# Kernel tuning notes

Measured on AMD Instinct MI355X. Metric: run time of the kernel, lower is better.

The kernel has to match this reference:

```python
import jax, jax.numpy as jnp
from jax import lax
import numpy as np

NDIM = 256
BATCH = 65536
NROT = NDIM * (NDIM - 1) // 2  # comb(ndim, 2) = 32640


def _givens_mat(rots, ii, jj, ndim):
    """Product G_last @ ... @ G_1 of Givens rotations in combinations order.

    Left-multiplying by G(i, j, theta) only modifies rows i and j, so we apply
    each rotation as a rank-2 row update instead of a full matmul (same math
    as the original `plane_rot_mat @ mat` loop).
    """
    def step(mat, carry):
        i, j, th = carry
        c = jnp.cos(th)
        s = jnp.sin(th)
        ri = mat[i]
        rj = mat[j]
        mat = mat.at[i].set(c * ri - s * rj)
        mat = mat.at[j].set(s * ri + c * rj)
        return mat, None

    mat0 = jnp.eye(ndim, dtype=jnp.complex64)
    mat, _ = lax.scan(step, mat0, (ii, jj, rots))
    return mat


def setup_inputs() -> dict:
    key = jax.random.key(0)
    k1, k2, k3, k4 = jax.random.split(key, 4)
    x = jax.random.normal(k1, (BATCH, NDIM), dtype=jnp.float32)
    rots1 = 0.1 * jax.random.normal(k2, (NROT,), dtype=jnp.float32)
    phases = 0.1 * jax.random.normal(k3, (NDIM,), dtype=jnp.float32)
    rots2 = 0.1 * jax.random.normal(k4, (NROT,), dtype=jnp.float32)
    return {"x": x, "rots1": rots1, "phases": phases, "rots2": rots2}


def reference(x, rots1, phases, rots2):
    ndim = x.shape[1]
    # np.triu_indices(ndim, 1) enumerates (i, j) pairs in the same row-major
    # order as itertools.combinations(range(ndim), 2).
    ii_np, jj_np = np.triu_indices(ndim, k=1)
    ii = jnp.asarray(ii_np, dtype=jnp.int32)
    jj = jnp.asarray(jj_np, dtype=jnp.int32)

    # vector_norm: row-wise L2 normalization
    xn = x / jnp.linalg.norm(x, axis=1, keepdims=True)
    xc = xn.astype(jnp.complex64)

    # rot1: y = x @ M1.T with M1 = G_last @ ... @ G_1
    M1 = _givens_mat(rots1, ii, jj, ndim)
    y = xc @ M1.T

    # phase_transforms: x @ diag(exp(i*phases)) == elementwise phase multiply
    y = y * jnp.exp(1j * phases)

    # rot2
    M2 = _givens_mat(rots2, ii, jj, ndim)
    y = y @ M2.T

    # measure: |.|^2
    return jnp.abs(y) ** 2
```

## Files before the change

### kernel.cpp

```cpp
#include <hip/hip_runtime.h>
#include <stdint.h>
#include <math.h>

#define NDIM 256
#define BATCH 65536
#define NROT 32640

typedef float  f32x4 __attribute__((ext_vector_type(4)));
typedef short  s16x8 __attribute__((ext_vector_type(8)));
typedef unsigned int u32x4 __attribute__((ext_vector_type(4)));
typedef unsigned int u32x2 __attribute__((ext_vector_type(2)));

static __device__ __forceinline__ unsigned short f2bf(float f) {
    unsigned int u = __float_as_uint(f);
    u += 0x7fffu + ((u >> 16) & 1u);
    return (unsigned short)(u >> 16);
}
static __device__ __forceinline__ float bf2f(unsigned short h) {
    return __uint_as_float(((unsigned)h) << 16);
}

static __device__ __forceinline__ void split4(f32x4 v, u32x2* hi, u32x2* lo) {
    unsigned short h[4], l[4];
    #pragma unroll
    for (int i = 0; i < 4; i++) {
        h[i] = f2bf(v[i]);
        l[i] = f2bf(v[i] - bf2f(h[i]));
    }
    *hi = (u32x2){ (unsigned)h[0] | ((unsigned)h[1] << 16),
                   (unsigned)h[2] | ((unsigned)h[3] << 16) };
    *lo = (u32x2){ (unsigned)l[0] | ((unsigned)l[1] << 16),
                   (unsigned)l[2] | ((unsigned)l[3] << 16) };
}
static __device__ __forceinline__ void split8(const float* v, u32x4* hi, u32x4* lo) {
    unsigned short h[8], l[8];
    #pragma unroll
    for (int i = 0; i < 8; i++) {
        h[i] = f2bf(v[i]);
        l[i] = f2bf(v[i] - bf2f(h[i]));
    }
    *hi = (u32x4){ (unsigned)h[0] | ((unsigned)h[1] << 16),
                   (unsigned)h[2] | ((unsigned)h[3] << 16),
                   (unsigned)h[4] | ((unsigned)h[5] << 16),
                   (unsigned)h[6] | ((unsigned)h[7] << 16) };
    *lo = (u32x4){ (unsigned)l[0] | ((unsigned)l[1] << 16),
                   (unsigned)l[2] | ((unsigned)l[3] << 16),
                   (unsigned)l[4] | ((unsigned)l[5] << 16),
                   (unsigned)l[6] | ((unsigned)l[7] << 16) };
}

static __device__ __forceinline__ int sweep_bound(int k, int pblk) {
    int target = k * (NROT / pblk);
    int best = 0, bd = 0x7fffffff;
    for (int i = 0; i <= 256; i += 4) {
        int pre = i * 255 - (i * (i - 1)) / 2;
        int d = pre - target; d = (d < 0) ? -d : d;
        if (d < bd) { bd = d; best = i; }
    }
    return best;
}

__global__ __launch_bounds__(256) void k_cs(const float* __restrict__ r1,
                                            const float* __restrict__ r2,
                                            float2* __restrict__ cs) {
    int i = blockIdx.x * 256 + threadIdx.x;
    float th = (i < NROT) ? r1[i] : r2[i - NROT];
    float sv, cv; sincosf(th, &sv, &cv);
    cs[i] = make_float2(cv, sv);
}

__global__ __launch_bounds__(64) void k_blocks(const float2* __restrict__ cs,
                                               float* __restrict__ bmats, int pblk) {
    __shared__ float colb[264 * 64];
    __shared__ float2 csb[256 * 4];
    __shared__ float2 tri[24 * 6];

    const int t = threadIdx.x;
    const int bid = blockIdx.x;
    const int chunk = bid & 3;
    const int b = (bid >> 2) % pblk;
    const int set = (bid >> 2) / pblk;
    const int col0 = chunk * 64;
    const float2* cst = cs + (size_t)set * NROT;

    const int s0 = sweep_bound(b, pblk);
    const int s1 = sweep_bound(b + 1, pblk);
    const int ngroups = (s1 - s0) >> 2;

    {
        const f32x4 z = {0.f, 0.f, 0.f, 0.f};
        #pragma unroll 11
        for (int q = 0; q < 66; q++)
            *(f32x4*)&colb[(q * 64 + t) * 4] = z;
        colb[(col0 + t) * 64 + t] = 1.0f;
    }

    for (int k = t; k < ngroups * 6; k += 64) {
        int g = k / 6, q = k - g * 6;
        int a  = (q < 3) ? 0 : ((q < 5) ? 1 : 2);
        int bb = (q < 3) ? (q + 1) : ((q < 5) ? (q - 1) : 3);
        int m0 = s0 + g * 4;
        int m = m0 + a;
        int base = m * 255 - (m * (m - 1)) / 2;
        tri[k] = cst[base - m - 1 + m0 + bb];
    }

    float2 gv[16];
    {
        const int m0g = s0;
        int offg[4];
        #pragma unroll
        for (int a = 0; a < 4; a++) {
            int m = m0g + a;
            offg[a] = m * 255 - (m * (m - 1)) / 2 - m - 1;
        }
        #pragma unroll
        for (int it = 0; it < 16; it++) {
            int k = t + it * 64;
            int jj = k >> 2, a = k & 3;
            int j = m0g + 4 + jj;
            gv[it] = (j < 256) ? cst[offg[a] + j] : make_float2(1.f, 0.f);
        }
        #pragma unroll
        for (int it = 0; it < 16; it++)
            csb[t + it * 64] = gv[it];
    }

    for (int g = 0; g < ngroups; g++) {
        const int m0 = s0 + g * 4;
        const int n_j = 252 - m0;
        const int n_p = (n_j > 0) ? ((n_j + 7) & ~7) : 0;
        const float* csbuf = (const float*)&csb[0];

        const bool have_next = (g + 1 < ngroups);
        if (have_next) {
            const int m0g = m0 + 4;
            int offg[4];
            #pragma unroll
            for (int a = 0; a < 4; a++) {
                int m = m0g + a;
                offg[a] = m * 255 - (m * (m - 1)) / 2 - m - 1;
            }
            #pragma unroll
            for (int it = 0; it < 16; it++) {
                int k = t + it * 64;
                int jj = k >> 2, a = k & 3;
                int j = m0g + 4 + jj;
                gv[it] = (j < 256) ? cst[offg[a] + j] : make_float2(1.f, 0.f);
            }
        }

        float u0 = colb[(m0 + 0) * 64 + t];
        float u1 = colb[(m0 + 1) * 64 + t];
        float u2 = colb[(m0 + 2) * 64 + t];
        float u3 = colb[(m0 + 3) * 64 + t];

        {
            float2 cv; float nr;
            cv = tri[g * 6 + 0]; nr = cv.y * u0 + cv.x * u1; u0 = cv.x * u0 - cv.y * u1; u1 = nr;
            cv = tri[g * 6 + 1]; nr = cv.y * u0 + cv.x * u2; u0 = cv.x * u0 - cv.y * u2; u2 = nr;
            cv = tri[g * 6 + 2]; nr = cv.y * u0 + cv.x * u3; u0 = cv.x * u0 - cv.y * u3; u3 = nr;
            cv = tri[g * 6 + 3]; nr = cv.y * u1 + cv.x * u2; u1 = cv.x * u1 - cv.y * u2; u2 = nr;
            cv = tri[g * 6 + 4]; nr = cv.y * u1 + cv.x * u3; u1 = cv.x * u1 - cv.y * u3; u3 = nr;
            cv = tri[g * 6 + 5]; nr = cv.y * u2 + cv.x * u3; u2 = cv.x * u2 - cv.y * u3; u3 = nr;
        }

        if (n_p > 0) {
            float rbuf[8];
            f32x4 abuf[8][2];
            #pragma unroll
            for (int p = 0; p < 8; p++) {
                rbuf[p] = colb[(m0 + 4 + p) * 64 + t];
                abuf[p][0] = *(const f32x4*)&csbuf[p * 8 + 0];
                abuf[p][1] = *(const f32x4*)&csbuf[p * 8 + 4];
            }
            for (int c = 0; c < n_p; c += 8) {
                #pragma unroll
                for (int p = 0; p < 8; p++) {
                    const int j = m0 + 4 + c + p;
                    float r = rbuf[p];
                    f32x4 A01 = abuf[p][0], A23 = abuf[p][1];
                    int jn = j + 8; jn = (jn < 263) ? jn : 263;
                    int cn = c + p + 8; cn = (cn < n_p) ? cn : (n_p - 1);
                    rbuf[p] = colb[jn * 64 + t];
                    abuf[p][0] = *(const f32x4*)&csbuf[cn * 8 + 0];
                    abuf[p][1] = *(const f32x4*)&csbuf[cn * 8 + 4];
                    float nr;
                    nr = A01[1] * u0 + A01[0] * r; u0 = A01[0] * u0 - A01[1] * r; r = nr;
                    nr = A01[3] * u1 + A01[2] * r; u1 = A01[2] * u1 - A01[3] * r; r = nr;
                    nr = A23[1] * u2 + A23[0] * r; u2 = A23[0] * u2 - A23[1] * r; r = nr;
                    nr = A23[3] * u3 + A23[2] * r; u3 = A23[2] * u3 - A23[3] * r; r = nr;
                    colb[j * 64 + t] = r;
                }
            }
        }
        colb[(m0 + 0) * 64 + t] = u0;
        colb[(m0 + 1) * 64 + t] = u1;
        colb[(m0 + 2) * 64 + t] = u2;
        colb[(m0 + 3) * 64 + t] = u3;

        if (have_next) {
            #pragma unroll
            for (int it = 0; it < 16; it++)
                csb[t + it * 64] = gv[it];
        }
    }

    float* outm = bmats + (size_t)(set * pblk + b) * 65536;
    for (int r = 0; r < 256; r++)
        outm[(size_t)r * 256 + col0 + t] = colb[r * 64 + t];
}

static __device__ __forceinline__ void xnorm_item(const float* __restrict__ xg,
                                                  unsigned short* __restrict__ xbf,
                                                  int id, int tid) {
    const int w = tid >> 6, lane = tid & 63;
    const int r0 = id * 64;
    #pragma unroll 2
    for (int p = 0; p < 16; p++) {
        int row = r0 + p * 4 + w;
        f32x4 v = *(const f32x4*)&xg[(size_t)row * 256 + lane * 4];
        float s = v[0] * v[0] + v[1] * v[1] + v[2] * v[2] + v[3] * v[3];
        #pragma unroll
        for (int off = 32; off; off >>= 1) s += __shfl_xor(s, off, 64);
        float sc = 1.0f / sqrtf(s);
        unsigned short h0 = f2bf(v[0] * sc), h1 = f2bf(v[1] * sc);
        unsigned short h2 = f2bf(v[2] * sc), h3 = f2bf(v[3] * sc);
        u32x2 pk = { (unsigned)h0 | ((unsigned)h1 << 16),
                     (unsigned)h2 | ((unsigned)h3 << 16) };
        *(u32x2*)&xbf[(size_t)row * 256 + lane * 4] = pk;
    }
}

#define TB 2560

static __device__ __forceinline__ int bslot(int row, int s) {
    return row * 40 + ((s ^ ((row >> 3) & 3)) << 3);
}

static __device__ __forceinline__ void tile_issueA(const float* __restrict__ Am,
                                                   int tr, int kb, int tid,
                                                   f32x4 va[2]) {
    #pragma unroll
    for (int it = 0; it < 2; it++) {
        int flat = tid + it * 256;
        int r = flat >> 3, c4 = flat & 7;
        va[it] = *(const f32x4*)&Am[(size_t)(tr * 64 + r) * 256 + kb * 32 + c4 * 4];
    }
}
static __device__ __forceinline__ void tile_issueB(const float* __restrict__ Bm,
                                                   int tc, int kb, int bn, int bkq,
                                                   float vb[8]) {
    #pragma unroll
    for (int i = 0; i < 8; i++)
        vb[i] = Bm[(size_t)(kb * 32 + bkq * 8 + i) * 256 + tc * 64 + bn];
}
static __device__ __forceinline__ void tile_commit(unsigned short* __restrict__ Ahi,
                                                   unsigned short* __restrict__ Alo,
                                                   unsigned short* __restrict__ Bhi,
                                                   unsigned short* __restrict__ Blo,
                                                   int tid, int bn, int bkq,
                                                   const f32x4 va[2], const float vb[8]) {
    #pragma unroll
    for (int it = 0; it < 2; it++) {
        int flat = tid + it * 256;
        int r = flat >> 3, c4 = flat & 7;
        u32x2 hi, lo; split4(va[it], &hi, &lo);
        *(u32x2*)&Ahi[r * 40 + c4 * 4] = hi;
        *(u32x2*)&Alo[r * 40 + c4 * 4] = lo;
    }
    u32x4 hi8, lo8; split8(vb, &hi8, &lo8);
    *(u32x4*)&Bhi[bslot(bn, bkq)] = hi8;
    *(u32x4*)&Blo[bslot(bn, bkq)] = lo8;
}
static __device__ __forceinline__ void tile_mfma(const unsigned short* __restrict__ Ahi,
                                                 const unsigned short* __restrict__ Alo,
                                                 const unsigned short* __restrict__ Bhi,
                                                 const unsigned short* __restrict__ Blo,
                                                 int mh, int nh, int l15, int lq,
                                                 f32x4 acc[2][2]) {
    s16x8 ah[2], al[2], bh[2], bl[2];
    #pragma unroll
    for (int tm = 0; tm < 2; tm++) {
        ah[tm] = *(const s16x8*)&Ahi[(mh + tm * 16 + l15) * 40 + lq * 8];
        al[tm] = *(const s16x8*)&Alo[(mh + tm * 16 + l15) * 40 + lq * 8];
    }
    #pragma unroll
    for (int tn = 0; tn < 2; tn++) {
        bh[tn] = *(const s16x8*)&Bhi[bslot(nh + tn * 16 + l15, lq)];
        bl[tn] = *(const s16x8*)&Blo[bslot(nh + tn * 16 + l15, lq)];
    }
    #pragma unroll
    for (int tm = 0; tm < 2; tm++)
        #pragma unroll
        for (int tn = 0; tn < 2; tn++) {
            acc[tm][tn] = __builtin_amdgcn_mfma_f32_16x16x32_bf16(ah[tm], bh[tn], acc[tm][tn], 0, 0, 0);
            acc[tm][tn] = __builtin_amdgcn_mfma_f32_16x16x32_bf16(ah[tm], bl[tn], acc[tm][tn], 0, 0, 0);
            acc[tm][tn] = __builtin_amdgcn_mfma_f32_16x16x32_bf16(al[tm], bh[tn], acc[tm][tn], 0, 0, 0);
        }
}

static __device__ void combine_tile(const float* __restrict__ src,
                                    float* __restrict__ dst,
                                    int half, int pblk, int bx, int by, int tid,
                                    unsigned short* Ahi, unsigned short* Alo,
                                    unsigned short* Bhi, unsigned short* Blo) {
    const int set = by / half, pidx = by % half;
    const int stride = pblk / (2 * half);
    const int s0A = sweep_bound((2 * pidx + 1) * stride, pblk);
    const float* Am = src + (size_t)(set * 2 * half + 2 * pidx + 1) * 65536;
    const float* Bm = src + (size_t)(set * 2 * half + 2 * pidx) * 65536;
    float* Dm = dst + (size_t)(set * half + pidx) * 65536;
    const int tr = bx >> 2, tc = bx & 3;

    if (tr * 64 + 64 <= s0A) {
        #pragma unroll
        for (int it = 0; it < 4; it++) {
            int flat = tid + it * 256;
            int r = flat >> 4, c4 = flat & 15;
            size_t idx = (size_t)(tr * 64 + r) * 256 + tc * 64 + c4 * 4;
            *(f32x4*)&Dm[idx] = *(const f32x4*)&Bm[idx];
        }
        return;
    }
    const int kb0 = (tr * 64 >= s0A) ? (s0A >> 5) : 0;

    const int lane = tid & 63, w = tid >> 6;
    const int mh = (w >> 1) * 32, nh = (w & 1) * 32;
    const int l15 = lane & 15, lq = lane >> 4;
    const int bn = tid & 63, bkq = tid >> 6;

    f32x4 acc[2][2];
    #pragma unroll
    for (int i = 0; i < 2; i++)
        #pragma unroll
        for (int j = 0; j < 2; j++) acc[i][j] = (f32x4){0.f, 0.f, 0.f, 0.f};

    f32x4 vaE[2], vaO[2]; float vbE[8], vbO[8];
    tile_issueA(Am, tr, kb0, tid, vaE);
    tile_issueB(Bm, tc, kb0, bn, bkq, vbE);
    if (kb0 + 1 < 8) {
        tile_issueA(Am, tr, kb0 + 1, tid, vaO);
        tile_issueB(Bm, tc, kb0 + 1, bn, bkq, vbO);
    }

    for (int kb = kb0; kb < 8; kb++) {
        const int cur = (kb - kb0) & 1;
        if (cur == 0) {
            tile_commit(Ahi, Alo, Bhi, Blo, tid, bn, bkq, vaE, vbE);
            __syncthreads();
            if (kb + 2 < 8) {
                tile_issueA(Am, tr, kb + 2, tid, vaE);
                tile_issueB(Bm, tc, kb + 2, bn, bkq, vbE);
            }
        } else {
            tile_commit(Ahi, Alo, Bhi, Blo, tid, bn, bkq, vaO, vbO);
            __syncthreads();
            if (kb + 2 < 8) {
                tile_issueA(Am, tr, kb + 2, tid, vaO);
                tile_issueB(Bm, tc, kb + 2, bn, bkq, vbO);
            }
        }
        tile_mfma(Ahi, Alo, Bhi, Blo, mh, nh, l15, lq, acc);
        __syncthreads();
    }
    #pragma unroll
    for (int tm = 0; tm < 2; tm++)
        #pragma unroll
        for (int tn = 0; tn < 2; tn++)
            #pragma unroll
            for (int r = 0; r < 4; r++)
                Dm[(size_t)(tr * 64 + mh + tm * 16 + lq * 4 + r) * 256
                   + tc * 64 + nh + tn * 16 + l15] = acc[tm][tn][r];
}

static __device__ void abt_tile(const float* __restrict__ mats,
                                const float* __restrict__ phases,
                                unsigned short* __restrict__ abtp,
                                int bx, int v, int tid,
                                unsigned short* Ahi, unsigned short* Alo,
                                unsigned short* Bhi, unsigned short* Blo) {
    const float* Am = mats + 65536;
    const float* Bm = mats;
    const int tr = bx >> 2, tc = bx & 3;

    const int lane = tid & 63, w = tid >> 6;
    const int mh = (w >> 1) * 32, nh = (w & 1) * 32;
    const int l15 = lane & 15, lq = lane >> 4;
    const int bn = tid & 63, bkq = tid >> 6;

    f32x4 acc[2][2];
    #pragma unroll
    for (int i = 0; i < 2; i++)
        #pragma unroll
        for (int j = 0; j < 2; j++) acc[i][j] = (f32x4){0.f, 0.f, 0.f, 0.f};

    auto issueBs = [&](int kb, float vb[8]) {
        #pragma unroll
        for (int i = 0; i < 8; i++) {
            int kg = kb * 32 + bkq * 8 + i;
            float ph = phases[kg];
            float sc = v ? sinf(ph) : cosf(ph);
            vb[i] = Bm[(size_t)kg * 256 + tc * 64 + bn] * sc;
        }
    };

    f32x4 vaE[2], vaO[2]; float vbE[8], vbO[8];
    tile_issueA(Am, tr, 0, tid, vaE); issueBs(0, vbE);
    tile_issueA(Am, tr, 1, tid, vaO); issueBs(1, vbO);

    for (int kb = 0; kb < 8; kb++) {
        const int cur = kb & 1;
        if (cur == 0) {
            tile_commit(Ahi, Alo, Bhi, Blo, tid, bn, bkq, vaE, vbE);
            __syncthreads();
            if (kb + 2 < 8) { tile_issueA(Am, tr, kb + 2, tid, vaE); issueBs(kb + 2, vbE); }
        } else {
            tile_commit(Ahi, Alo, Bhi, Blo, tid, bn, bkq, vaO, vbO);
            __syncthreads();
            if (kb + 2 < 8) { tile_issueA(Am, tr, kb + 2, tid, vaO); issueBs(kb + 2, vbO); }
        }
        tile_mfma(Ahi, Alo, Bhi, Blo, mh, nh, l15, lq, acc);
        __syncthreads();
    }
    #pragma unroll
    for (int tm = 0; tm < 2; tm++)
        #pragma unroll
        for (int tn = 0; tn < 2; tn++)
            #pragma unroll
            for (int r = 0; r < 4; r++)
                abtp[(size_t)(v * 256 + tr * 64 + mh + tm * 16 + lq * 4 + r) * 256
                     + tc * 64 + nh + tn * 16 + l15] = f2bf(acc[tm][tn][r]);
}

__global__ __launch_bounds__(256) void k_combine(const float* __restrict__ src,
                                                 float* __restrict__ dst,
                                                 int half, int pblk,
                                                 const float* __restrict__ xg,
                                                 unsigned short* __restrict__ xbf) {
    __shared__ unsigned short Ahi[TB], Alo[TB], Bhi[TB], Blo[TB];
    const int by = blockIdx.y, tid = threadIdx.x;
    if (by >= 2 * half) {
        xnorm_item(xg, xbf, (by - 2 * half) * 16 + blockIdx.x, tid);
        return;
    }
    combine_tile(src, dst, half, pblk, blockIdx.x, by, tid, Ahi, Alo, Bhi, Blo);
}

__global__ __launch_bounds__(256) void k_abt(const float* __restrict__ mats,
                                             const float* __restrict__ phases,
                                             unsigned short* __restrict__ abtp) {
    __shared__ unsigned short Ahi[TB], Alo[TB], Bhi[TB], Blo[TB];
    abt_tile(mats, phases, abtp, blockIdx.x, blockIdx.y, threadIdx.x,
             Ahi, Alo, Bhi, Blo);
}

__global__ __launch_bounds__(256) void k_norm(const float* __restrict__ x,
                                              float* __restrict__ invn) {
    const int row = blockIdx.x * 4 + (threadIdx.x >> 6);
    const int lane = threadIdx.x & 63;
    f32x4 v = *(const f32x4*)&x[(size_t)row * 256 + lane * 4];
    float s = v[0] * v[0] + v[1] * v[1] + v[2] * v[2] + v[3] * v[3];
    for (int off = 32; off; off >>= 1) s += __shfl_xor(s, off, 64);
    if (lane == 0) invn[row] = 1.0f / sqrtf(s);
}

#define BKP 136
__global__ __launch_bounds__(256) void k_gemm_bf(const unsigned short* __restrict__ xbf,
                                                 const unsigned short* __restrict__ abt,
                                                 float* __restrict__ out) {
    __shared__ unsigned short As[128 * BKP];
    __shared__ unsigned short Bs[128 * BKP];
    const int tid = threadIdx.x;
    const int l  = blockIdx.y * 4 + blockIdx.x;
    const int L  = (l & 7) * 256 + (l >> 3);
    const int cb = L & 3;
    const int rb = L >> 2;
    const int lane = tid & 63, w = tid >> 6;

    f32x4 acc[16];
    #pragma unroll
    for (int i = 0; i < 16; i++) acc[i] = (f32x4){0.f, 0.f, 0.f, 0.f};

    int rA[8], cA[8], grB[8];
    #pragma unroll
    for (int it = 0; it < 8; it++) {
        int flat = tid + it * 256;
        rA[it] = flat >> 4; cA[it] = flat & 15;
        int r = rA[it];
        grB[it] = (r < 64) ? (cb * 64 + r) : (256 + cb * 64 + (r - 64));
    }

    u32x4 pa[8], pb[8];
    #pragma unroll
    for (int it = 0; it < 8; it++) {
        pa[it] = *(const u32x4*)&xbf[(size_t)(rb * 128 + rA[it]) * 256 + cA[it] * 8];
        pb[it] = *(const u32x4*)&abt[(size_t)grB[it] * 256 + cA[it] * 8];
    }
    #pragma unroll
    for (int it = 0; it < 8; it++) {
        *(u32x4*)&As[rA[it] * BKP + cA[it] * 8] = pa[it];
        *(u32x4*)&Bs[rA[it] * BKP + cA[it] * 8] = pb[it];
    }
    __syncthreads();
    #pragma unroll
    for (int it = 0; it < 8; it++) {
        pa[it] = *(const u32x4*)&xbf[(size_t)(rb * 128 + rA[it]) * 256 + 128 + cA[it] * 8];
        pb[it] = *(const u32x4*)&abt[(size_t)grB[it] * 256 + 128 + cA[it] * 8];
    }

    auto compute = [&]() {
        #pragma unroll
        for (int ks = 0; ks < 4; ks++) {
            const int k0 = ks * 32 + (lane >> 4) * 8;
            s16x8 a[2], b[8];
            #pragma unroll
            for (int tm = 0; tm < 2; tm++)
                a[tm] = *(const s16x8*)&As[(w * 32 + tm * 16 + (lane & 15)) * BKP + k0];
            #pragma unroll
            for (int tn = 0; tn < 8; tn++)
                b[tn] = *(const s16x8*)&Bs[(tn * 16 + (lane & 15)) * BKP + k0];
            #pragma unroll
            for (int tm = 0; tm < 2; tm++)
                #pragma unroll
                for (int tn = 0; tn < 8; tn++)
                    acc[tm * 8 + tn] = __builtin_amdgcn_mfma_f32_16x16x32_bf16(
                        a[tm], b[tn], acc[tm * 8 + tn], 0, 0, 0);
        }
    };
    compute();
    __syncthreads();
    #pragma unroll
    for (int it = 0; it < 8; it++) {
        *(u32x4*)&As[rA[it] * BKP + cA[it] * 8] = pa[it];
        *(u32x4*)&Bs[rA[it] * BKP + cA[it] * 8] = pb[it];
    }
    __syncthreads();
    compute();

    const int qr = lane >> 4, c = lane & 15;
    #pragma unroll
    for (int tm = 0; tm < 2; tm++) {
        #pragma unroll
        for (int tn = 0; tn < 4; tn++) {
            f32x4 p = acc[tm * 8 + tn];
            f32x4 q = acc[tm * 8 + tn + 4];
            #pragma unroll
            for (int r = 0; r < 4; r++) {
                int m = w * 32 + tm * 16 + qr * 4 + r;
                out[(size_t)(rb * 128 + m) * 256 + cb * 64 + tn * 16 + c] =
                    p[r] * p[r] + q[r] * q[r];
            }
        }
    }
}

__global__ __launch_bounds__(256) void k_gemm_f32(const float* __restrict__ x,
                                                  const unsigned short* __restrict__ abt,
                                                  const float* __restrict__ invn,
                                                  float* __restrict__ out) {
    __shared__ unsigned short As[128 * BKP];
    __shared__ unsigned short Bs[128 * BKP];
    const int tid = threadIdx.x;
    const int l  = blockIdx.y * 4 + blockIdx.x;
    const int L  = (l & 7) * 256 + (l >> 3);
    const int cb = L & 3;
    const int rb = L >> 2;
    const int lane = tid & 63, w = tid >> 6;

    f32x4 acc[16];
    #pragma unroll
    for (int i = 0; i < 16; i++) acc[i] = (f32x4){0.f, 0.f, 0.f, 0.f};

    for (int kb = 0; kb < 2; kb++) {
        __syncthreads();
        #pragma unroll
        for (int it = 0; it < 16; it++) {
            int flat = tid + it * 256;
            int r = flat >> 5, c4 = flat & 31;
            f32x4 v = *(const f32x4*)&x[(size_t)(rb * 128 + r) * 256 + kb * 128 + c4 * 4];
            float sc = invn[rb * 128 + r];
            v[0] *= sc; v[1] *= sc; v[2] *= sc; v[3] *= sc;
            unsigned short h0 = f2bf(v[0]), h1 = f2bf(v[1]);
            unsigned short h2 = f2bf(v[2]), h3 = f2bf(v[3]);
            u32x2 pk = { (unsigned)h0 | ((unsigned)h1 << 16),
                         (unsigned)h2 | ((unsigned)h3 << 16) };
            *(u32x2*)&As[r * BKP + c4 * 4] = pk;
        }
        #pragma unroll
        for (int it = 0; it < 8; it++) {
            int flat = tid + it * 256;
            int r = flat >> 4, c8 = flat & 15;
            int gr = (r < 64) ? (cb * 64 + r) : (256 + cb * 64 + (r - 64));
            u32x4 vv = *(const u32x4*)&abt[(size_t)gr * 256 + kb * 128 + c8 * 8];
            *(u32x4*)&Bs[r * BKP + c8 * 8] = vv;
        }
        __syncthreads();
        #pragma unroll
        for (int ks = 0; ks < 4; ks++) {
            const int k0 = ks * 32 + (lane >> 4) * 8;
            s16x8 a[2], b[8];
            #pragma unroll
            for (int tm = 0; tm < 2; tm++)
                a[tm] = *(const s16x8*)&As[(w * 32 + tm * 16 + (lane & 15)) * BKP + k0];
            #pragma unroll
            for (int tn = 0; tn < 8; tn++)
                b[tn] = *(const s16x8*)&Bs[(tn * 16 + (lane & 15)) * BKP + k0];
            #pragma unroll
            for (int tm = 0; tm < 2; tm++)
                #pragma unroll
                for (int tn = 0; tn < 8; tn++)
                    acc[tm * 8 + tn] = __builtin_amdgcn_mfma_f32_16x16x32_bf16(
                        a[tm], b[tn], acc[tm * 8 + tn], 0, 0, 0);
        }
    }

    const int qr = lane >> 4, c = lane & 15;
    #pragma unroll
    for (int tm = 0; tm < 2; tm++) {
        #pragma unroll
        for (int tn = 0; tn < 4; tn++) {
            f32x4 p = acc[tm * 8 + tn];
            f32x4 q = acc[tm * 8 + tn + 4];
            #pragma unroll
            for (int r = 0; r < 4; r++) {
                int m = w * 32 + tm * 16 + qr * 4 + r;
                out[(size_t)(rb * 128 + m) * 256 + cb * 64 + tn * 16 + c] =
                    p[r] * p[r] + q[r] * q[r];
            }
        }
    }
}

extern "C" void kernel_launch(void* const* d_in, const int* in_sizes, int n_in,
                              void* d_out, int out_size, void* d_ws, size_t ws_size,
                              hipStream_t stream) {
    (void)in_sizes; (void)n_in; (void)out_size;
    const float* x      = (const float*)d_in[0];
    const float* rots1  = (const float*)d_in[1];
    const float* phases = (const float*)d_in[2];
    const float* rots2  = (const float*)d_in[3];
    float* out = (float*)d_out;
    char* ws = (char*)d_ws;

    const size_t MAT = 262144;
    int pblk = 64;
    while (pblk > 16 &&
           (size_t)3 * pblk * MAT + 2 * MAT + (size_t)BATCH * 512 > ws_size)
        pblk >>= 1;
    const size_t offA   = 0;
    const size_t offB   = offA + (size_t)2 * pblk * MAT;
    const size_t offABT = offB + (size_t)pblk * MAT;
    const size_t offINV = offABT + MAT;
    const size_t offXBF = offINV + MAT;
    const bool use_xbf = (offXBF + (size_t)BATCH * 512) <= ws_size;

    float*          A    = (float*)(ws + offA);
    float*          B    = (float*)(ws + offB);
    unsigned short* abt  = (unsigned short*)(ws + offABT);
    float*          invn = (float*)(ws + offINV);
    unsigned short* xbf  = (unsigned short*)(ws + offXBF);
    float2*         cs   = (float2*)(ws + offB);

    k_cs<<<(2 * NROT) / 256, 256, 0, stream>>>(rots1, rots2, cs);
    k_blocks<<<8 * pblk, 64, 0, stream>>>(cs, A, pblk);

    float* srcp = A; float* dstp = B;
    bool first = true;
    for (int half = pblk / 2; half >= 1; half >>= 1) {
        const int xny = (first && use_xbf) ? 64 : 0;
        k_combine<<<dim3(16, 2 * half + xny), 256, 0, stream>>>(srcp, dstp, half,
                                                                pblk, x, xbf);
        float* tmp = srcp; srcp = dstp; dstp = tmp;
        first = false;
    }
    k_abt<<<dim3(16, 2), 256, 0, stream>>>(srcp, phases, abt);

    if (use_xbf) {
        k_gemm_bf<<<dim3(4, BATCH / 128), 256, 0, stream>>>(xbf, abt, out);
    } else {
        k_norm<<<BATCH / 4, 256, 0, stream>>>(x, invn);
        k_gemm_f32<<<dim3(4, BATCH / 128), 256, 0, stream>>>(x, abt, invn, out);
    }
}
```

Measured before the change: 279.8 us.

## Split-K the ABT matrix product across blocks with separate reduction kernel

Replaces the 32-block k_abt kernel, which loops serially over 8 K-chunks, with a split-K version. It launches 256 blocks that each compute one K-chunk partial product into the free ping-pong buffer, then a small reduction kernel sums the 8 partials and converts them to bf16. The aim is to fill more compute units in this small serial stage. The cost is an extra launch plus writing and reading 8 fp32 partial matrices through global memory.

```diff
diff --git a/kernel.cpp b/kernel.cpp
--- a/kernel.cpp
+++ b/kernel.cpp
@@ -374,65 +374,6 @@
                    + tc * 64 + nh + tn * 16 + l15] = acc[tm][tn][r];
 }
 
-static __device__ void abt_tile(const float* __restrict__ mats,
-                                const float* __restrict__ phases,
-                                unsigned short* __restrict__ abtp,
-                                int bx, int v, int tid,
-                                unsigned short* Ahi, unsigned short* Alo,
-                                unsigned short* Bhi, unsigned short* Blo) {
-    const float* Am = mats + 65536;
-    const float* Bm = mats;
-    const int tr = bx >> 2, tc = bx & 3;
-
-    const int lane = tid & 63, w = tid >> 6;
-    const int mh = (w >> 1) * 32, nh = (w & 1) * 32;
-    const int l15 = lane & 15, lq = lane >> 4;
-    const int bn = tid & 63, bkq = tid >> 6;
-
-    f32x4 acc[2][2];
-    #pragma unroll
-    for (int i = 0; i < 2; i++)
-        #pragma unroll
-        for (int j = 0; j < 2; j++) acc[i][j] = (f32x4){0.f, 0.f, 0.f, 0.f};
-
-    auto issueBs = [&](int kb, float vb[8]) {
-        #pragma unroll
-        for (int i = 0; i < 8; i++) {
-            int kg = kb * 32 + bkq * 8 + i;
-            float ph = phases[kg];
-            float sc = v ? sinf(ph) : cosf(ph);
-            vb[i] = Bm[(size_t)kg * 256 + tc * 64 + bn] * sc;
-        }
-    };
-
-    f32x4 vaE[2], vaO[2]; float vbE[8], vbO[8];
-    tile_issueA(Am, tr, 0, tid, vaE); issueBs(0, vbE);
-    tile_issueA(Am, tr, 1, tid, vaO); issueBs(1, vbO);
-
-    for (int kb = 0; kb < 8; kb++) {
-        const int cur = kb & 1;
-        if (cur == 0) {
-            tile_commit(Ahi, Alo, Bhi, Blo, tid, bn, bkq, vaE, vbE);
-            __syncthreads();
-            if (kb + 2 < 8) { tile_issueA(Am, tr, kb + 2, tid, vaE); issueBs(kb + 2, vbE); }
-        } else {
-            tile_commit(Ahi, Alo, Bhi, Blo, tid, bn, bkq, vaO, vbO);
-            __syncthreads();
-            if (kb + 2 < 8) { tile_issueA(Am, tr, kb + 2, tid, vaO); issueBs(kb + 2, vbO); }
-        }
-        tile_mfma(Ahi, Alo, Bhi, Blo, mh, nh, l15, lq, acc);
-        __syncthreads();
-    }
-    #pragma unroll
-    for (int tm = 0; tm < 2; tm++)
-        #pragma unroll
-        for (int tn = 0; tn < 2; tn++)
-            #pragma unroll
-            for (int r = 0; r < 4; r++)
-                abtp[(size_t)(v * 256 + tr * 64 + mh + tm * 16 + lq * 4 + r) * 256
-                     + tc * 64 + nh + tn * 16 + l15] = f2bf(acc[tm][tn][r]);
-}
-
 __global__ __launch_bounds__(256) void k_combine(const float* __restrict__ src,
                                                  float* __restrict__ dst,
                                                  int half, int pblk,
@@ -447,12 +388,66 @@
     combine_tile(src, dst, half, pblk, blockIdx.x, by, tid, Ahi, Alo, Bhi, Blo);
 }
 
-__global__ __launch_bounds__(256) void k_abt(const float* __restrict__ mats,
-                                             const float* __restrict__ phases,
-                                             unsigned short* __restrict__ abtp) {
+__global__ __launch_bounds__(256) void k_abt_part(const float* __restrict__ mats,
+                                                  const float* __restrict__ phases,
+                                                  float* __restrict__ part) {
     __shared__ unsigned short Ahi[TB], Alo[TB], Bhi[TB], Blo[TB];
-    abt_tile(mats, phases, abtp, blockIdx.x, blockIdx.y, threadIdx.x,
-             Ahi, Alo, Bhi, Blo);
+    const float* Am = mats + 65536;
+    const float* Bm = mats;
+    const int tid = threadIdx.x;
+    const int bx = blockIdx.x;
+    const int v  = blockIdx.y;
+    const int kb = blockIdx.z;
+    const int tr = bx >> 2, tc = bx & 3;
+
+    const int lane = tid & 63, w = tid >> 6;
+    const int mh = (w >> 1) * 32, nh = (w & 1) * 32;
+    const int l15 = lane & 15, lq = lane >> 4;
+    const int bn = tid & 63, bkq = tid >> 6;
+
+    f32x4 va[2]; float vb[8];
+    tile_issueA(Am, tr, kb, tid, va);
+    #pragma unroll
+    for (int i = 0; i < 8; i++) {
+        int kg = kb * 32 + bkq * 8 + i;
+        float ph = phases[kg];
+        float sc = v ? sinf(ph) : cosf(ph);
+        vb[i] = Bm[(size_t)kg * 256 + tc * 64 + bn] * sc;
+    }
+
+    f32x4 acc[2][2];
+    #pragma unroll
+    for (int i = 0; i < 2; i++)
+        #pragma unroll
+        for (int j = 0; j < 2; j++) acc[i][j] = (f32x4){0.f, 0.f, 0.f, 0.f};
+
+    tile_commit(Ahi, Alo, Bhi, Blo, tid, bn, bkq, va, vb);
+    __syncthreads();
+    tile_mfma(Ahi, Alo, Bhi, Blo, mh, nh, l15, lq, acc);
+
+    float* pp = part + (size_t)(kb * 2 + v) * 65536;
+    #pragma unroll
+    for (int tm = 0; tm < 2; tm++)
+        #pragma unroll
+        for (int tn = 0; tn < 2; tn++)
+            #pragma unroll
+            for (int r = 0; r < 4; r++)
+                pp[(size_t)(tr * 64 + mh + tm * 16 + lq * 4 + r) * 256
+                   + tc * 64 + nh + tn * 16 + l15] = acc[tm][tn][r];
+}
+
+__global__ __launch_bounds__(256) void k_abt_red(const float* __restrict__ part,
+                                                 unsigned short* __restrict__ abt) {
+    const int e = (blockIdx.x * 256 + threadIdx.x) * 4;
+    f32x4 s = {0.f, 0.f, 0.f, 0.f};
+    #pragma unroll
+    for (int kz = 0; kz < 8; kz++)
+        s += *(const f32x4*)&part[(size_t)kz * 131072 + e];
+    unsigned short h0 = f2bf(s[0]), h1 = f2bf(s[1]);
+    unsigned short h2 = f2bf(s[2]), h3 = f2bf(s[3]);
+    u32x2 pk = { (unsigned)h0 | ((unsigned)h1 << 16),
+                 (unsigned)h2 | ((unsigned)h3 << 16) };
+    *(u32x2*)&abt[e] = pk;
 }
 
 __global__ __launch_bounds__(256) void k_norm(const float* __restrict__ x,
@@ -674,7 +669,8 @@
         float* tmp = srcp; srcp = dstp; dstp = tmp;
         first = false;
     }
-    k_abt<<<dim3(16, 2), 256, 0, stream>>>(srcp, phases, abt);
+    k_abt_part<<<dim3(16, 2, 8), 256, 0, stream>>>(srcp, phases, dstp);
+    k_abt_red<<<128, 256, 0, stream>>>(dstp, abt);
 
     if (use_xbf) {
         k_gemm_bf<<<dim3(4, BATCH / 128), 256, 0, stream>>>(xbf, abt, out);
```

Measured after the change: 262.1 us. 6.3% less time.
